# Kernel tuning notes

Hardware: AMD Instinct MI355X
Metric: run time of the kernel (lower is better)

## Reference

```python
import jax, jax.numpy as jnp
import numpy as np

B, T, K = 128, 2048, 96  # batch, seq_len, num_tags


def setup_inputs() -> dict:
    key = jax.random.key(0)
    k1, k2, k3, k4, k5 = jax.random.split(key, 5)
    logits = jax.random.normal(k1, (B, T, K), dtype=jnp.float32)
    labels = jax.random.randint(k2, (B, T), 0, K)
    mask = jnp.ones((B, T), dtype=bool)
    # learned CRF parameters
    transitions = jax.random.normal(k3, (K, K), dtype=jnp.float32) * 0.1
    start_transitions = jax.random.normal(k4, (K,), dtype=jnp.float32) * 0.1
    end_transitions = jax.random.normal(k5, (K,), dtype=jnp.float32) * 0.1
    return {
        "logits": logits,
        "labels": labels,
        "mask": mask,
        "transitions": transitions,
        "start_transitions": start_transitions,
        "end_transitions": end_transitions,
    }


def _log_partition(logits, maskf, transitions, start_transitions, end_transitions):
    # forward algorithm over time via scan; logits: [B,T,K]
    em = jnp.transpose(logits, (1, 0, 2))   # [T,B,K]
    mk = jnp.transpose(maskf, (1, 0))       # [T,B]
    alpha0 = start_transitions[None, :] + em[0]  # [B,K]

    def step(alpha, x):
        emit_t, m_t = x
        # alpha[b,i] + transitions[i,j] + emit[b,j] -> logsumexp over i
        inner = alpha[:, :, None] + transitions[None, :, :] + emit_t[:, None, :]
        new = jax.nn.logsumexp(inner, axis=1)
        alpha = jnp.where(m_t[:, None] > 0, new, alpha)
        return alpha, None

    alpha, _ = jax.lax.scan(step, alpha0, (em[1:], mk[1:]))
    return jax.nn.logsumexp(alpha + end_transitions[None, :], axis=1)  # [B]


def _joint_score(logits, labels, maskf, mask, transitions, start_transitions, end_transitions):
    b = jnp.arange(logits.shape[0])
    emit = jnp.take_along_axis(logits, labels[..., None], axis=2)[..., 0]  # [B,T]
    emit_sum = jnp.sum(emit * maskf, axis=1)
    trans = transitions[labels[:, :-1], labels[:, 1:]]                     # [B,T-1]
    trans_sum = jnp.sum(trans * maskf[:, 1:], axis=1)
    seq_len = jnp.sum(mask.astype(jnp.int32), axis=1)
    last_tags = labels[b, seq_len - 1]
    return start_transitions[labels[:, 0]] + emit_sum + trans_sum + end_transitions[last_tags]


def reference(logits, labels, mask, transitions, start_transitions, end_transitions):
    maskf = mask.astype(logits.dtype)
    logZ = _log_partition(logits, maskf, transitions, start_transitions, end_transitions)
    score = _joint_score(logits, labels, maskf, mask, transitions, start_transitions, end_transitions)
    log_lik = jnp.sum(score - logZ)
    return -log_lik
```

## Files before the change

kernel.cpp:

```cpp
#include <hip/hip_runtime.h>
#include <math.h>

#define B_ 128
#define T_ 2048
#define K_ 96
#define NC 256
#define CH 8
#define WARM 6
#define GRP 16
#define SP 100
#define LOGZ_BLOCKS (8 * NC)
#define SCORE_BLOCKS 256

typedef __attribute__((ext_vector_type(8))) short short8;
typedef __attribute__((ext_vector_type(4))) float float4v;
union U8 { unsigned u[4]; short8 v; };

__device__ __forceinline__ unsigned pack_trunc(float lo, float hi) {
    return __builtin_amdgcn_perm(__builtin_bit_cast(unsigned, hi),
                                 __builtin_bit_cast(unsigned, lo), 0x07060302u);
}
__device__ __forceinline__ unsigned short bf16_rne(float x) {
    unsigned u = __builtin_bit_cast(unsigned, x);
    u += 0x7FFFu + ((u >> 16) & 1u);
    return (unsigned short)(u >> 16);
}
__device__ __forceinline__ float wave_reduce_sum(float x) {
#pragma unroll
    for (int off = 1; off < 64; off <<= 1) x += __shfl_xor(x, off, 64);
    return x;
}

__device__ __forceinline__ void crf_step(
    int k, int len, float* __restrict__ Sw, int lo, int q,
    const short8 (&Bf)[6][3], const float* __restrict__ eptr,
    float4 (&eb)[6], float4 (&cvN)[6], float &acc, float &R, float &logR)
{
    acc += logR;
    float4 pr[6];
#pragma unroll
    for (int i = 0; i < 6; ++i) {
        float4 e = eb[i], cc = cvN[i];
        pr[i] = make_float4((cc.x * R) * __expf(e.x), (cc.y * R) * __expf(e.y),
                            (cc.z * R) * __expf(e.z), (cc.w * R) * __expf(e.w));
    }

    short8 Af[3];
#pragma unroll
    for (int f = 0; f < 3; ++f) {
        float4 v0 = pr[2 * f], v1 = pr[2 * f + 1];
        U8 ua;
        ua.u[0] = pack_trunc(v0.x, v0.y);
        ua.u[1] = pack_trunc(v0.z, v0.w);
        ua.u[2] = pack_trunc(v1.x, v1.y);
        ua.u[3] = pack_trunc(v1.z, v1.w);
        Af[f] = ua.v;
    }

    if (k + 2 <= len) {
        const float* p = eptr + (size_t)(k + 1) * K_;
        eb[0] = *(const float4*)(p);
        eb[1] = *(const float4*)(p + 4);
        eb[2] = *(const float4*)(p + 32);
        eb[3] = *(const float4*)(p + 36);
        eb[4] = *(const float4*)(p + 64);
        eb[5] = *(const float4*)(p + 68);
    }

    float4v Cv[6];
#pragma unroll
    for (int nt = 0; nt < 6; ++nt) {
        float4v cz = {0.f, 0.f, 0.f, 0.f};
        cz = __builtin_amdgcn_mfma_f32_16x16x32_bf16(Af[0], Bf[nt][0], cz, 0, 0, 0);
        cz = __builtin_amdgcn_mfma_f32_16x16x32_bf16(Af[1], Bf[nt][1], cz, 0, 0, 0);
        Cv[nt] = __builtin_amdgcn_mfma_f32_16x16x32_bf16(Af[2], Bf[nt][2], cz, 0, 0, 0);
    }

    float c00 = __shfl(Cv[0][0], 0, 64);
    R = __builtin_amdgcn_rcpf(c00);
    logR = __logf(c00);

#pragma unroll
    for (int nt = 0; nt < 6; ++nt)
#pragma unroll
        for (int r = 0; r < 4; ++r)
            Sw[(4 * q + r) * SP + 16 * nt + lo] = Cv[nt][r];

#pragma unroll
    for (int f = 0; f < 3; ++f) {
        cvN[2 * f]     = *(const float4*)&Sw[lo * SP + 32 * f + 8 * q];
        cvN[2 * f + 1] = *(const float4*)&Sw[lo * SP + 32 * f + 8 * q + 4];
    }
}

__device__ __forceinline__ float measureM(const float4 (&cvN)[6], float acc,
                                          float logR) {
    float mx = 0.f;
#pragma unroll
    for (int i = 0; i < 6; ++i) {
        float4 v = cvN[i];
        mx = fmaxf(mx, fmaxf(fmaxf(v.x, v.y), fmaxf(v.z, v.w)));
    }
    mx = fmaxf(mx, __shfl_xor(mx, 16, 64));
    mx = fmaxf(mx, __shfl_xor(mx, 32, 64));
    return __logf(mx) + acc + logR;
}

__global__ void __launch_bounds__(64, 2) crf_fused_kernel(
    const float* __restrict__ logits, const int* __restrict__ labels,
    const float* __restrict__ trans, const float* __restrict__ startT,
    const float* __restrict__ endT, float* __restrict__ out)
{
    __shared__ __align__(16) float Sw[GRP * SP];
    const int tid = threadIdx.x;

    if (blockIdx.x >= LOGZ_BLOCKS) {
        int gid = (blockIdx.x - LOGZ_BLOCKS) * 64 + tid;
        float acc2 = 0.f;
        for (int i = gid; i < B_ * T_; i += SCORE_BLOCKS * 64) {
            int b = i >> 11, t = i & (T_ - 1);
            const int* lab = labels + (size_t)b * T_;
            int lt = lab[t];
            acc2 += logits[((size_t)b * T_ + t) * K_ + lt];
            acc2 += (t > 0) ? trans[lab[t - 1] * K_ + lt] : startT[lt];
            if (t == T_ - 1) acc2 += endT[lt];
        }
        acc2 = wave_reduce_sum(acc2);
        if (tid == 0) atomicAdd(out, -acc2);
        return;
    }

    const int lane = tid, lo = lane & 15, q = lane >> 4;
    const int W = blockIdx.x;
    const int c = W & (NC - 1);
    const int grp = W >> 8;
    const int ts = (c == 0) ? 0 : (CH * c - WARM);
    const int len = (c == 0) ? CH : ((c < NC - 1) ? (WARM + CH) : (WARM + CH - 1));

    short8 Bf[6][3];
#pragma unroll
    for (int nt = 0; nt < 6; ++nt)
#pragma unroll
        for (int kf = 0; kf < 3; ++kf) {
            U8 ub;
#pragma unroll
            for (int p = 0; p < 4; ++p) {
                int k0 = 32 * kf + 8 * q + 2 * p;
                int n = 16 * nt + lo;
                unsigned l = bf16_rne(__expf(trans[(size_t)k0 * K_ + n]));
                unsigned h = bf16_rne(__expf(trans[(size_t)(k0 + 1) * K_ + n]));
                ub.u[p] = l | (h << 16);
            }
            Bf[nt][kf] = ub.v;
        }

    float4 cvN[6];
    if (c == 0) {
#pragma unroll
        for (int f = 0; f < 3; ++f) {
            int k0 = 32 * f + 8 * q;
            float4 s0 = *(const float4*)(startT + k0);
            float4 s1 = *(const float4*)(startT + k0 + 4);
            cvN[2 * f]     = make_float4(__expf(s0.x), __expf(s0.y), __expf(s0.z), __expf(s0.w));
            cvN[2 * f + 1] = make_float4(__expf(s1.x), __expf(s1.y), __expf(s1.z), __expf(s1.w));
        }
    } else {
        float4 one = make_float4(1.f, 1.f, 1.f, 1.f);
#pragma unroll
        for (int i = 0; i < 6; ++i) cvN[i] = one;
    }

    const float* eptr = logits + ((size_t)(grp * GRP + lo) * T_ + ts) * K_ + 8 * q;
    float4 eb0[6], eb1[6];
    {
        const float* p0 = eptr;
        eb0[0] = *(const float4*)(p0);      eb0[1] = *(const float4*)(p0 + 4);
        eb0[2] = *(const float4*)(p0 + 32); eb0[3] = *(const float4*)(p0 + 36);
        eb0[4] = *(const float4*)(p0 + 64); eb0[5] = *(const float4*)(p0 + 68);
        const float* p1 = eptr + K_;
        eb1[0] = *(const float4*)(p1);      eb1[1] = *(const float4*)(p1 + 4);
        eb1[2] = *(const float4*)(p1 + 32); eb1[3] = *(const float4*)(p1 + 36);
        eb1[4] = *(const float4*)(p1 + 64); eb1[5] = *(const float4*)(p1 + 68);
    }

    float acc = 0.f, R = 1.f, logR = 0.f, Mwarm = 0.f;
    int k = 1;
    if (c != 0) {
#pragma unroll 1
        for (int n2 = 0; n2 < WARM / 2; ++n2) {
            crf_step(k, len, Sw, lo, q, Bf, eptr, eb0, cvN, acc, R, logR); ++k;
            crf_step(k, len, Sw, lo, q, Bf, eptr, eb1, cvN, acc, R, logR); ++k;
        }
        Mwarm = measureM(cvN, acc, 0.f);
    }

    const int pairs = (len - k + 1) >> 1;
#pragma unroll 1
    for (int n2 = 0; n2 < pairs; ++n2) {
        crf_step(k, len, Sw, lo, q, Bf, eptr, eb0, cvN, acc, R, logR); ++k;
        crf_step(k, len, Sw, lo, q, Bf, eptr, eb1, cvN, acc, R, logR); ++k;
    }
    if (k <= len) { crf_step(k, len, Sw, lo, q, Bf, eptr, eb0, cvN, acc, R, logR); ++k; }

    float contrib;
    if (c < NC - 1) {
        contrib = measureM(cvN, acc, 0.f) - Mwarm;
    } else {
        const float* pe = eptr + (size_t)len * K_;
        float xv[24];
#pragma unroll
        for (int f = 0; f < 3; ++f) {
            int k0 = 32 * f + 8 * q;
            float4 e0 = *(const float4*)(pe + 32 * f);
            float4 e1 = *(const float4*)(pe + 32 * f + 4);
            float4 d0 = *(const float4*)(endT + k0);
            float4 d1 = *(const float4*)(endT + k0 + 4);
            float4 c0 = cvN[2 * f], c1 = cvN[2 * f + 1];
            xv[f * 8 + 0] = __logf(c0.x) + e0.x + d0.x;
            xv[f * 8 + 1] = __logf(c0.y) + e0.y + d0.y;
            xv[f * 8 + 2] = __logf(c0.z) + e0.z + d0.z;
            xv[f * 8 + 3] = __logf(c0.w) + e0.w + d0.w;
            xv[f * 8 + 4] = __logf(c1.x) + e1.x + d1.x;
            xv[f * 8 + 5] = __logf(c1.y) + e1.y + d1.y;
            xv[f * 8 + 6] = __logf(c1.z) + e1.z + d1.z;
            xv[f * 8 + 7] = __logf(c1.w) + e1.w + d1.w;
        }
        float m2 = -1e30f;
#pragma unroll
        for (int i = 0; i < 24; ++i) m2 = fmaxf(m2, xv[i]);
        m2 = fmaxf(m2, __shfl_xor(m2, 16, 64));
        m2 = fmaxf(m2, __shfl_xor(m2, 32, 64));
        float p2 = 0.f;
#pragma unroll
        for (int i = 0; i < 24; ++i) p2 += __expf(xv[i] - m2);
        p2 += __shfl_xor(p2, 16, 64);
        p2 += __shfl_xor(p2, 32, 64);
        contrib = m2 + __logf(p2) + acc - Mwarm;
    }

    float cvv = (lane < 16) ? contrib : 0.f;
    cvv = wave_reduce_sum(cvv);
    if (lane == 0) atomicAdd(out, cvv);
}

extern "C" void kernel_launch(void* const* d_in, const int* in_sizes, int n_in,
                              void* d_out, int out_size, void* d_ws, size_t ws_size,
                              hipStream_t stream)
{
    const float* logits = (const float*)d_in[0];
    const int*   labels = (const int*)d_in[1];
    const float* trans  = (const float*)d_in[3];
    const float* startT = (const float*)d_in[4];
    const float* endT   = (const float*)d_in[5];
    float* out = (float*)d_out;

    hipMemsetAsync(out, 0, sizeof(float), stream);
    hipLaunchKernelGGL(crf_fused_kernel, dim3(LOGZ_BLOCKS + SCORE_BLOCKS),
                       dim3(64), 0, stream,
                       logits, labels, trans, startT, endT, out);
}
```

Measured before the change: 205.9 us.

## Interleave two time-chunk streams per wave to hide step latency

Each wave now processes two adjacent time chunks (A and B) of the CRF forward recursion instead of one, halving the number of logZ blocks. Steps of the two independent chains are interleaved so MFMA, LDS and exp latency of one chain can overlap with the other, and the transition-matrix fragments are loaded once for both. This raises register pressure with two sets of state and emission buffers and double LDS scratch, and adds per-step predication for the skip and warm-up bookkeeping.

```diff
diff --git a/kernel.cpp b/kernel.cpp
--- a/kernel.cpp
+++ b/kernel.cpp
@@ -9,8 +9,10 @@
 #define WARM 6
 #define GRP 16
 #define SP 100
-#define LOGZ_BLOCKS (8 * NC)
+#define NWAVE 1024
+#define LOGZ_BLOCKS NWAVE
 #define SCORE_BLOCKS 256
+#define JMAX 14
 
 typedef __attribute__((ext_vector_type(8))) short short8;
 typedef __attribute__((ext_vector_type(4))) float float4v;
@@ -93,8 +95,7 @@
     }
 }
 
-__device__ __forceinline__ float measureM(const float4 (&cvN)[6], float acc,
-                                          float logR) {
+__device__ __forceinline__ float measureM(const float4 (&cvN)[6], float acc) {
     float mx = 0.f;
 #pragma unroll
     for (int i = 0; i < 6; ++i) {
@@ -103,7 +104,59 @@
     }
     mx = fmaxf(mx, __shfl_xor(mx, 16, 64));
     mx = fmaxf(mx, __shfl_xor(mx, 32, 64));
-    return __logf(mx) + acc + logR;
+    return __logf(mx) + acc;
+}
+
+__device__ __forceinline__ void preload(const float* __restrict__ eptr, int skip,
+                                        float4 (&b0)[6], float4 (&b1)[6]) {
+    int o0 = (skip & 1) ? 1 : 0;
+    int o1 = 1 - o0;
+    const float* p0 = eptr + (size_t)o0 * K_;
+    b0[0] = *(const float4*)(p0);      b0[1] = *(const float4*)(p0 + 4);
+    b0[2] = *(const float4*)(p0 + 32); b0[3] = *(const float4*)(p0 + 36);
+    b0[4] = *(const float4*)(p0 + 64); b0[5] = *(const float4*)(p0 + 68);
+    const float* p1 = eptr + (size_t)o1 * K_;
+    b1[0] = *(const float4*)(p1);      b1[1] = *(const float4*)(p1 + 4);
+    b1[2] = *(const float4*)(p1 + 32); b1[3] = *(const float4*)(p1 + 36);
+    b1[4] = *(const float4*)(p1 + 64); b1[5] = *(const float4*)(p1 + 68);
+}
+
+__device__ __forceinline__ float stream_tail(
+    int c, const float4 (&cvN)[6], float acc, float Mwarm,
+    const float* __restrict__ eptr, int len, const float* __restrict__ endT,
+    int lo, int q)
+{
+    if (c < NC - 1) return measureM(cvN, acc) - Mwarm;
+    const float* pe = eptr + (size_t)len * K_;
+    float xv[24];
+#pragma unroll
+    for (int f = 0; f < 3; ++f) {
+        int k0 = 32 * f + 8 * q;
+        float4 e0 = *(const float4*)(pe + 32 * f);
+        float4 e1 = *(const float4*)(pe + 32 * f + 4);
+        float4 d0 = *(const float4*)(endT + k0);
+        float4 d1 = *(const float4*)(endT + k0 + 4);
+        float4 c0 = cvN[2 * f], c1 = cvN[2 * f + 1];
+        xv[f * 8 + 0] = __logf(c0.x) + e0.x + d0.x;
+        xv[f * 8 + 1] = __logf(c0.y) + e0.y + d0.y;
+        xv[f * 8 + 2] = __logf(c0.z) + e0.z + d0.z;
+        xv[f * 8 + 3] = __logf(c0.w) + e0.w + d0.w;
+        xv[f * 8 + 4] = __logf(c1.x) + e1.x + d1.x;
+        xv[f * 8 + 5] = __logf(c1.y) + e1.y + d1.y;
+        xv[f * 8 + 6] = __logf(c1.z) + e1.z + d1.z;
+        xv[f * 8 + 7] = __logf(c1.w) + e1.w + d1.w;
+    }
+    float m2 = -1e30f;
+#pragma unroll
+    for (int i = 0; i < 24; ++i) m2 = fmaxf(m2, xv[i]);
+    m2 = fmaxf(m2, __shfl_xor(m2, 16, 64));
+    m2 = fmaxf(m2, __shfl_xor(m2, 32, 64));
+    float p2 = 0.f;
+#pragma unroll
+    for (int i = 0; i < 24; ++i) p2 += __expf(xv[i] - m2);
+    p2 += __shfl_xor(p2, 16, 64);
+    p2 += __shfl_xor(p2, 32, 64);
+    return m2 + __logf(p2) + acc - Mwarm;
 }
 
 __global__ void __launch_bounds__(64, 2) crf_fused_kernel(
@@ -111,7 +164,7 @@
     const float* __restrict__ trans, const float* __restrict__ startT,
     const float* __restrict__ endT, float* __restrict__ out)
 {
-    __shared__ __align__(16) float Sw[GRP * SP];
+    __shared__ __align__(16) float Sw[2][GRP * SP];
     const int tid = threadIdx.x;
 
     if (blockIdx.x >= LOGZ_BLOCKS) {
@@ -132,10 +185,15 @@
 
     const int lane = tid, lo = lane & 15, q = lane >> 4;
     const int W = blockIdx.x;
-    const int c = W & (NC - 1);
-    const int grp = W >> 8;
-    const int ts = (c == 0) ? 0 : (CH * c - WARM);
-    const int len = (c == 0) ? CH : ((c < NC - 1) ? (WARM + CH) : (WARM + CH - 1));
+    const int grp = W >> 7;
+    const int w = W & 127;
+    const int cA = 2 * w, cB = 2 * w + 1;
+
+    const int tsA = (cA == 0) ? 0 : (CH * cA - WARM);
+    const int lenA = (cA == 0) ? CH : ((cA < NC - 1) ? (WARM + CH) : (WARM + CH - 1));
+    const int tsB = CH * cB - WARM;
+    const int lenB = (cB < NC - 1) ? (WARM + CH) : (WARM + CH - 1);
+    const int skipA = JMAX - lenA, skipB = JMAX - lenB;
 
     short8 Bf[6][3];
 #pragma unroll
@@ -154,89 +212,61 @@
             Bf[nt][kf] = ub.v;
         }
 
-    float4 cvN[6];
-    if (c == 0) {
+    float4 cvNA[6], cvNB[6];
+    float4 one = make_float4(1.f, 1.f, 1.f, 1.f);
+    if (cA == 0) {
 #pragma unroll
         for (int f = 0; f < 3; ++f) {
             int k0 = 32 * f + 8 * q;
             float4 s0 = *(const float4*)(startT + k0);
             float4 s1 = *(const float4*)(startT + k0 + 4);
-            cvN[2 * f]     = make_float4(__expf(s0.x), __expf(s0.y), __expf(s0.z), __expf(s0.w));
-            cvN[2 * f + 1] = make_float4(__expf(s1.x), __expf(s1.y), __expf(s1.z), __expf(s1.w));
+            cvNA[2 * f]     = make_float4(__expf(s0.x), __expf(s0.y), __expf(s0.z), __expf(s0.w));
+            cvNA[2 * f + 1] = make_float4(__expf(s1.x), __expf(s1.y), __expf(s1.z), __expf(s1.w));
         }
     } else {
-        float4 one = make_float4(1.f, 1.f, 1.f, 1.f);
-#pragma unroll
-        for (int i = 0; i < 6; ++i) cvN[i] = one;
-    }
-
-    const float* eptr = logits + ((size_t)(grp * GRP + lo) * T_ + ts) * K_ + 8 * q;
-    float4 eb0[6], eb1[6];
-    {
-        const float* p0 = eptr;
-        eb0[0] = *(const float4*)(p0);      eb0[1] = *(const float4*)(p0 + 4);
-        eb0[2] = *(const float4*)(p0 + 32); eb0[3] = *(const float4*)(p0 + 36);
-        eb0[4] = *(const float4*)(p0 + 64); eb0[5] = *(const float4*)(p0 + 68);
-        const float* p1 = eptr + K_;
-        eb1[0] = *(const float4*)(p1);      eb1[1] = *(const float4*)(p1 + 4);
-        eb1[2] = *(const float4*)(p1 + 32); eb1[3] = *(const float4*)(p1 + 36);
-        eb1[4] = *(const float4*)(p1 + 64); eb1[5] = *(const float4*)(p1 + 68);
-    }
-
-    float acc = 0.f, R = 1.f, logR = 0.f, Mwarm = 0.f;
-    int k = 1;
-    if (c != 0) {
+#pragma unroll
+        for (int i = 0; i < 6; ++i) cvNA[i] = one;
+    }
+#pragma unroll
+    for (int i = 0; i < 6; ++i) cvNB[i] = one;
+
+    const float* eptrA = logits + ((size_t)(grp * GRP + lo) * T_ + tsA) * K_ + 8 * q;
+    const float* eptrB = logits + ((size_t)(grp * GRP + lo) * T_ + tsB) * K_ + 8 * q;
+    float4 ebA0[6], ebA1[6], ebB0[6], ebB1[6];
+    preload(eptrA, skipA, ebA0, ebA1);
+    preload(eptrB, skipB, ebB0, ebB1);
+
+    float accA = 0.f, RA = 1.f, logRA = 0.f, MwarmA = 0.f;
+    float accB = 0.f, RB = 1.f, logRB = 0.f, MwarmB = 0.f;
+    int kA = 1, kB = 1;
+
 #pragma unroll 1
-        for (int n2 = 0; n2 < WARM / 2; ++n2) {
-            crf_step(k, len, Sw, lo, q, Bf, eptr, eb0, cvN, acc, R, logR); ++k;
-            crf_step(k, len, Sw, lo, q, Bf, eptr, eb1, cvN, acc, R, logR); ++k;
-        }
-        Mwarm = measureM(cvN, acc, 0.f);
-    }
-
-    const int pairs = (len - k + 1) >> 1;
-#pragma unroll 1
-    for (int n2 = 0; n2 < pairs; ++n2) {
-        crf_step(k, len, Sw, lo, q, Bf, eptr, eb0, cvN, acc, R, logR); ++k;
-        crf_step(k, len, Sw, lo, q, Bf, eptr, eb1, cvN, acc, R, logR); ++k;
-    }
-    if (k <= len) { crf_step(k, len, Sw, lo, q, Bf, eptr, eb0, cvN, acc, R, logR); ++k; }
-
-    float contrib;
-    if (c < NC - 1) {
-        contrib = measureM(cvN, acc, 0.f) - Mwarm;
-    } else {
-        const float* pe = eptr + (size_t)len * K_;
-        float xv[24];
-#pragma unroll
-        for (int f = 0; f < 3; ++f) {
-            int k0 = 32 * f + 8 * q;
-            float4 e0 = *(const float4*)(pe + 32 * f);
-            float4 e1 = *(const float4*)(pe + 32 * f + 4);
-            float4 d0 = *(const float4*)(endT + k0);
-            float4 d1 = *(const float4*)(endT + k0 + 4);
-            float4 c0 = cvN[2 * f], c1 = cvN[2 * f + 1];
-            xv[f * 8 + 0] = __logf(c0.x) + e0.x + d0.x;
-            xv[f * 8 + 1] = __logf(c0.y) + e0.y + d0.y;
-            xv[f * 8 + 2] = __logf(c0.z) + e0.z + d0.z;
-            xv[f * 8 + 3] = __logf(c0.w) + e0.w + d0.w;
-            xv[f * 8 + 4] = __logf(c1.x) + e1.x + d1.x;
-            xv[f * 8 + 5] = __logf(c1.y) + e1.y + d1.y;
-            xv[f * 8 + 6] = __logf(c1.z) + e1.z + d1.z;
-            xv[f * 8 + 7] = __logf(c1.w) + e1.w + d1.w;
-        }
-        float m2 = -1e30f;
-#pragma unroll
-        for (int i = 0; i < 24; ++i) m2 = fmaxf(m2, xv[i]);
-        m2 = fmaxf(m2, __shfl_xor(m2, 16, 64));
-        m2 = fmaxf(m2, __shfl_xor(m2, 32, 64));
-        float p2 = 0.f;
-#pragma unroll
-        for (int i = 0; i < 24; ++i) p2 += __expf(xv[i] - m2);
-        p2 += __shfl_xor(p2, 16, 64);
-        p2 += __shfl_xor(p2, 32, 64);
-        contrib = m2 + __logf(p2) + acc - Mwarm;
-    }
+    for (int it = 0; it < JMAX / 2; ++it) {
+        int j0 = 2 * it, j1 = 2 * it + 1;
+        if (j0 >= skipA) {
+            crf_step(kA, lenA, Sw[0], lo, q, Bf, eptrA, ebA0, cvNA, accA, RA, logRA);
+            if (kA == WARM && cA != 0) MwarmA = measureM(cvNA, accA);
+            ++kA;
+        }
+        if (j0 >= skipB) {
+            crf_step(kB, lenB, Sw[1], lo, q, Bf, eptrB, ebB0, cvNB, accB, RB, logRB);
+            if (kB == WARM) MwarmB = measureM(cvNB, accB);
+            ++kB;
+        }
+        if (j1 >= skipA) {
+            crf_step(kA, lenA, Sw[0], lo, q, Bf, eptrA, ebA1, cvNA, accA, RA, logRA);
+            if (kA == WARM && cA != 0) MwarmA = measureM(cvNA, accA);
+            ++kA;
+        }
+        if (j1 >= skipB) {
+            crf_step(kB, lenB, Sw[1], lo, q, Bf, eptrB, ebB1, cvNB, accB, RB, logRB);
+            if (kB == WARM) MwarmB = measureM(cvNB, accB);
+            ++kB;
+        }
+    }
+
+    float contrib = stream_tail(cA, cvNA, accA, MwarmA, eptrA, lenA, endT, lo, q)
+                  + stream_tail(cB, cvNB, accB, MwarmB, eptrB, lenB, endT, lo, q);
 
     float cvv = (lane < 16) ? contrib : 0.f;
     cvv = wave_reduce_sum(cvv);
```

Measured after the change: 188.5 us. -8.5%, faster.
